# Performance work log

Hardware: AMD Instinct MI355X
Metric: run time of the kernel (lower is better)

Reference implementation:

```python
import jax, jax.numpy as jnp
import numpy as np

K = 2  # top-k experts per token


def setup_inputs() -> dict:
    key = jax.random.key(0)
    k1, k2 = jax.random.split(key)
    B, S, H, E = 4, 4096, 4096, 64
    x = jax.random.normal(k1, (B, S, H), dtype=jnp.float32)
    gate_w = jax.random.normal(k2, (E, H), dtype=jnp.float32) * (H ** -0.5)
    return {"x": x, "gate_w": gate_w}


def reference(x, gate_w):
    # logits = x @ gate_w.T : [B, S, E]
    logits = jnp.einsum("bsh,eh->bse", x, gate_w)
    scores = jax.nn.softmax(logits, axis=-1)
    topk_scores, topk_idx = jax.lax.top_k(scores, K)  # [B, S, K]
    aux_loss = scores.mean() * 0.0
    z_loss = jnp.mean(logits.astype(jnp.float32) ** 2)
    return topk_idx, topk_scores, aux_loss, z_loss
```

## Files before the change

### kernel.cpp

```cpp
#include <hip/hip_runtime.h>
#include <hip/hip_bf16.h>


typedef __bf16  bf16x8  __attribute__((ext_vector_type(8)));
typedef float   f32x16  __attribute__((ext_vector_type(16)));

#define BS_TOK 16384
#define H_DIM  4096
#define E_DIM  64
#define MT     32
#define KWAVE  1024
#define NPANEL 16
#define WS_ZBUF_OFF (1536u << 10)

__device__ __forceinline__ void split3(float v, __bf16 &b0, __bf16 &b1, __bf16 &b2) {
    b0 = (__bf16)v;
    float r = v - (float)b0;
    b1 = (__bf16)r;
    float r2 = r - (float)b1;
    b2 = (__bf16)r2;
}

__device__ __forceinline__ void async_copy16(const float* gp, float* lp) {
    __builtin_amdgcn_global_load_lds(
        (const __attribute__((address_space(1))) void*)gp,
        (__attribute__((address_space(3))) void*)lp, 16, 0, 0);
}

__global__ void prep_w(const float* __restrict__ gw, bf16x8* __restrict__ wb) {
    int idx  = blockIdx.x * blockDim.x + threadIdx.x;
    int kb   = idx >> 7;
    int rem  = idx & 127;
    int nt   = rem >> 6;
    int lane = rem & 63;
    int n  = nt * 32 + (lane & 31);
    int kk = kb * 16 + ((lane >> 5) << 3);
    const float* p = gw + (size_t)n * H_DIM + kk;
    bf16x8 t0, t1, t2;
#pragma unroll
    for (int j = 0; j < 8; ++j) {
        __bf16 a, b, c;
        split3(p[j], a, b, c);
        t0[j] = a; t1[j] = b; t2[j] = c;
    }
    size_t fb = (size_t)(kb * 2 + nt) * 3;
    wb[(fb + 0) * 64 + lane] = t0;
    wb[(fb + 1) * 64 + lane] = t1;
    wb[(fb + 2) * 64 + lane] = t2;
}

__global__ __launch_bounds__(256, 2) void fused_router(
        const float* __restrict__ x, const bf16x8* __restrict__ wb,
        float* __restrict__ out, float* __restrict__ zbuf) {
    __shared__ float lds[16384];
    __shared__ float zsh[4];

    int tid = threadIdx.x;
    int w   = tid >> 6;
    int l   = tid & 63;
    int m0  = blockIdx.x * MT;
    float* sw = &lds[w * 4096];

    const float* gp[8];
#pragma unroll
    for (int r = 0; r < 8; ++r) {
        int g = 4 * r + (l >> 4);
        int c = (l & 15) ^ (g & 15);
        gp[r] = x + (size_t)(m0 + g) * H_DIM + w * KWAVE + c * 4;
    }

    f32x16 acc0, acc1;
#pragma unroll
    for (int r = 0; r < 16; ++r) { acc0[r] = 0.f; acc1[r] = 0.f; }

#pragma unroll
    for (int r = 0; r < 8; ++r) async_copy16(gp[r], sw + r * 256);

    int row = l & 31, half = l >> 5, rsw = row & 15;

    for (int p = 0; p < NPANEL; ++p) {
        __builtin_amdgcn_s_waitcnt(0x0F70);
        if (p + 1 < NPANEL) {
            float* dst = sw + ((p + 1) & 1) * 2048;
#pragma unroll
            for (int r = 0; r < 8; ++r)
                async_copy16(gp[r] + (p + 1) * 64, dst + r * 256);
        }
        const float* sb = sw + (p & 1) * 2048;
#pragma unroll
        for (int kk = 0; kk < 4; ++kk) {
            int c0 = kk * 4 + half * 2;
            float4 xa = *(const float4*)&sb[row * 64 + ((c0 ^ rsw) << 2)];
            float4 xb = *(const float4*)&sb[row * 64 + (((c0 + 1) ^ rsw) << 2)];
            bf16x8 a0, a1, a2;
            float xs[8] = {xa.x, xa.y, xa.z, xa.w, xb.x, xb.y, xb.z, xb.w};
#pragma unroll
            for (int j = 0; j < 8; ++j) {
                __bf16 h0, h1, h2;
                split3(xs[j], h0, h1, h2);
                a0[j] = h0; a1[j] = h1; a2[j] = h2;
            }
            int ks_abs = w * 64 + p * 4 + kk;
            const bf16x8* wp = wb + (size_t)ks_abs * 6 * 64 + l;
            bf16x8 b0 = wp[0*64], b1 = wp[1*64], b2 = wp[2*64];
            bf16x8 b3 = wp[3*64], b4 = wp[4*64], b5 = wp[5*64];
            acc0 = __builtin_amdgcn_mfma_f32_32x32x16_bf16(a0, b0, acc0, 0, 0, 0);
            acc0 = __builtin_amdgcn_mfma_f32_32x32x16_bf16(a1, b0, acc0, 0, 0, 0);
            acc0 = __builtin_amdgcn_mfma_f32_32x32x16_bf16(a2, b0, acc0, 0, 0, 0);
            acc0 = __builtin_amdgcn_mfma_f32_32x32x16_bf16(a0, b1, acc0, 0, 0, 0);
            acc0 = __builtin_amdgcn_mfma_f32_32x32x16_bf16(a1, b1, acc0, 0, 0, 0);
            acc0 = __builtin_amdgcn_mfma_f32_32x32x16_bf16(a0, b2, acc0, 0, 0, 0);
            acc1 = __builtin_amdgcn_mfma_f32_32x32x16_bf16(a0, b3, acc1, 0, 0, 0);
            acc1 = __builtin_amdgcn_mfma_f32_32x32x16_bf16(a1, b3, acc1, 0, 0, 0);
            acc1 = __builtin_amdgcn_mfma_f32_32x32x16_bf16(a2, b3, acc1, 0, 0, 0);
            acc1 = __builtin_amdgcn_mfma_f32_32x32x16_bf16(a0, b4, acc1, 0, 0, 0);
            acc1 = __builtin_amdgcn_mfma_f32_32x32x16_bf16(a1, b4, acc1, 0, 0, 0);
            acc1 = __builtin_amdgcn_mfma_f32_32x32x16_bf16(a0, b5, acc1, 0, 0, 0);
        }
    }

    __syncthreads();
    int col = l & 31;
#pragma unroll
    for (int r = 0; r < 16; ++r) {
        int mm = (r & 3) + ((r >> 2) << 3) + (half << 2);
        lds[w * 2048 + mm * 64 + col]      = acc0[r];
        lds[w * 2048 + mm * 64 + 32 + col] = acc1[r];
    }
    __syncthreads();

    float zacc = 0.f;
    for (int i = 0; i < 8; ++i) {
        int tl = w * 8 + i;
        float lg = lds[tl * 64 + l] + lds[2048 + tl * 64 + l]
                 + lds[4096 + tl * 64 + l] + lds[6144 + tl * 64 + l];
        zacc += lg * lg;

        float m = lg;
#pragma unroll
        for (int off = 32; off; off >>= 1) m = fmaxf(m, __shfl_xor(m, off));
        float e = expf(lg - m);
        float d = e;
#pragma unroll
        for (int off = 32; off; off >>= 1) d += __shfl_xor(d, off);
        float sc = e / d;

        float s1 = sc; int i1 = l;
#pragma unroll
        for (int off = 32; off; off >>= 1) {
            float os = __shfl_xor(s1, off); int oi = __shfl_xor(i1, off);
            if (os > s1 || (os == s1 && oi < i1)) { s1 = os; i1 = oi; }
        }
        float sm = (l == i1) ? -1.0f : sc;
        float s2 = sm; int i2 = l;
#pragma unroll
        for (int off = 32; off; off >>= 1) {
            float os = __shfl_xor(s2, off); int oi = __shfl_xor(i2, off);
            if (os > s2 || (os == s2 && oi < i2)) { s2 = os; i2 = oi; }
        }

        if (l == 0) {
            int t = m0 + tl;
            out[2 * t]                  = (float)i1;
            out[2 * t + 1]              = (float)i2;
            out[2 * BS_TOK + 2 * t]     = s1;
            out[2 * BS_TOK + 2 * t + 1] = s2;
        }
    }
#pragma unroll
    for (int off = 32; off; off >>= 1) zacc += __shfl_xor(zacc, off);
    if (l == 0) zsh[w] = zacc;
    __syncthreads();
    if (tid == 0)
        zbuf[blockIdx.x] = zsh[0] + zsh[1] + zsh[2] + zsh[3];
}

__global__ __launch_bounds__(256) void zreduce(const float* __restrict__ zbuf,
                                               float* __restrict__ out) {
    __shared__ float sh[4];
    int tid = threadIdx.x;
    float s = zbuf[tid] + zbuf[tid + 256];
#pragma unroll
    for (int off = 32; off; off >>= 1) s += __shfl_xor(s, off);
    if ((tid & 63) == 0) sh[tid >> 6] = s;
    __syncthreads();
    if (tid == 0) {
        out[4 * BS_TOK]     = 0.0f;
        out[4 * BS_TOK + 1] = (sh[0] + sh[1] + sh[2] + sh[3])
                              * (1.0f / (float)(BS_TOK * E_DIM));
    }
}

extern "C" void kernel_launch(void* const* d_in, const int* in_sizes, int n_in,
                              void* d_out, int out_size, void* d_ws, size_t ws_size,
                              hipStream_t stream) {
    const float* x  = (const float*)d_in[0];
    const float* gw = (const float*)d_in[1];
    float* out  = (float*)d_out;
    bf16x8* wb  = (bf16x8*)d_ws;
    float*  zbf = (float*)((char*)d_ws + WS_ZBUF_OFF);

    prep_w<<<128, 256, 0, stream>>>(gw, wb);
    fused_router<<<BS_TOK / MT, 256, 0, stream>>>(x, wb, out, zbf);
    zreduce<<<1, 256, 0, stream>>>(zbf, out);
}
```

Before: 410.4 us.

## Halve LDS panel size and software-prefetch weight fragments into registers

The x staging panel shrinks from 64 to 32 floats per row, halving LDS per block (64KB to 32KB) so more blocks can be resident. Weight fragments for the next panel are now loaded into a double-buffered register array (wA/wB) one panel ahead, instead of being loaded from global memory right before the MFMAs. The point is to hide weight-load latency and raise occupancy. The cost is more VGPRs (24 bf16x8 registers) and twice as many waitcnt sync points per wave. The single waitcnt(0x0F70) now also waits on the outstanding weight loads, which may serialize them.

```diff
diff --git a/kernel.cpp b/kernel.cpp
--- a/kernel.cpp
+++ b/kernel.cpp
@@ -10,7 +10,8 @@
 #define E_DIM  64
 #define MT     32
 #define KWAVE  1024
-#define NPANEL 16
+#define PANEL  32
+#define NPANEL (KWAVE / PANEL)
 #define WS_ZBUF_OFF (1536u << 10)
 
 __device__ __forceinline__ void split3(float v, __bf16 &b0, __bf16 &b1, __bf16 &b2) {
@@ -52,20 +53,20 @@
 __global__ __launch_bounds__(256, 2) void fused_router(
         const float* __restrict__ x, const bf16x8* __restrict__ wb,
         float* __restrict__ out, float* __restrict__ zbuf) {
-    __shared__ float lds[16384];
+    __shared__ float lds[8192];
     __shared__ float zsh[4];
 
     int tid = threadIdx.x;
     int w   = tid >> 6;
     int l   = tid & 63;
     int m0  = blockIdx.x * MT;
-    float* sw = &lds[w * 4096];
-
-    const float* gp[8];
-#pragma unroll
-    for (int r = 0; r < 8; ++r) {
-        int g = 4 * r + (l >> 4);
-        int c = (l & 15) ^ (g & 15);
+    float* sw = &lds[w * 2048];
+
+    const float* gp[4];
+#pragma unroll
+    for (int r = 0; r < 4; ++r) {
+        int g = 8 * r + (l >> 3);
+        int c = (l & 7) ^ (g & 7);
         gp[r] = x + (size_t)(m0 + g) * H_DIM + w * KWAVE + c * 4;
     }
 
@@ -73,25 +74,21 @@
 #pragma unroll
     for (int r = 0; r < 16; ++r) { acc0[r] = 0.f; acc1[r] = 0.f; }
 
-#pragma unroll
-    for (int r = 0; r < 8; ++r) async_copy16(gp[r], sw + r * 256);
-
-    int row = l & 31, half = l >> 5, rsw = row & 15;
-
-    for (int p = 0; p < NPANEL; ++p) {
-        __builtin_amdgcn_s_waitcnt(0x0F70);
-        if (p + 1 < NPANEL) {
-            float* dst = sw + ((p + 1) & 1) * 2048;
-#pragma unroll
-            for (int r = 0; r < 8; ++r)
-                async_copy16(gp[r] + (p + 1) * 64, dst + r * 256);
-        }
-        const float* sb = sw + (p & 1) * 2048;
-#pragma unroll
-        for (int kk = 0; kk < 4; ++kk) {
-            int c0 = kk * 4 + half * 2;
-            float4 xa = *(const float4*)&sb[row * 64 + ((c0 ^ rsw) << 2)];
-            float4 xb = *(const float4*)&sb[row * 64 + (((c0 + 1) ^ rsw) << 2)];
+    const bf16x8* wbl = wb + l;
+    auto loadW = [&](int p, bf16x8* wf) {
+        const bf16x8* wp = wbl + (size_t)(w * 64 + p * 2) * 6 * 64;
+#pragma unroll
+        for (int i = 0; i < 12; ++i) wf[i] = wp[i * 64];
+    };
+
+    int row = l & 31, half = l >> 5, rsw = (l & 31) & 7;
+
+    auto compute = [&](const float* sb, const bf16x8* wf) {
+#pragma unroll
+        for (int s = 0; s < 2; ++s) {
+            int c0 = s * 4 + half * 2;
+            float4 xa = *(const float4*)&sb[row * 32 + ((c0 ^ rsw) << 2)];
+            float4 xb = *(const float4*)&sb[row * 32 + (((c0 + 1) ^ rsw) << 2)];
             bf16x8 a0, a1, a2;
             float xs[8] = {xa.x, xa.y, xa.z, xa.w, xb.x, xb.y, xb.z, xb.w};
 #pragma unroll
@@ -100,10 +97,8 @@
                 split3(xs[j], h0, h1, h2);
                 a0[j] = h0; a1[j] = h1; a2[j] = h2;
             }
-            int ks_abs = w * 64 + p * 4 + kk;
-            const bf16x8* wp = wb + (size_t)ks_abs * 6 * 64 + l;
-            bf16x8 b0 = wp[0*64], b1 = wp[1*64], b2 = wp[2*64];
-            bf16x8 b3 = wp[3*64], b4 = wp[4*64], b5 = wp[5*64];
+            bf16x8 b0 = wf[s*6+0], b1 = wf[s*6+1], b2 = wf[s*6+2];
+            bf16x8 b3 = wf[s*6+3], b4 = wf[s*6+4], b5 = wf[s*6+5];
             acc0 = __builtin_amdgcn_mfma_f32_32x32x16_bf16(a0, b0, acc0, 0, 0, 0);
             acc0 = __builtin_amdgcn_mfma_f32_32x32x16_bf16(a1, b0, acc0, 0, 0, 0);
             acc0 = __builtin_amdgcn_mfma_f32_32x32x16_bf16(a2, b0, acc0, 0, 0, 0);
@@ -117,6 +112,28 @@
             acc1 = __builtin_amdgcn_mfma_f32_32x32x16_bf16(a1, b4, acc1, 0, 0, 0);
             acc1 = __builtin_amdgcn_mfma_f32_32x32x16_bf16(a0, b5, acc1, 0, 0, 0);
         }
+    };
+
+    bf16x8 wA[12], wB[12];
+    auto body = [&](int P, bf16x8* WC, bf16x8* WN) {
+        __builtin_amdgcn_s_waitcnt(0x0F70);
+        if (P + 1 < NPANEL) {
+            loadW(P + 1, WN);
+            float* dst = sw + ((P + 1) & 1) * 1024;
+#pragma unroll
+            for (int r = 0; r < 4; ++r)
+                async_copy16(gp[r] + (P + 1) * 32, dst + r * 256);
+        }
+        compute(sw + (P & 1) * 1024, WC);
+    };
+
+#pragma unroll
+    for (int r = 0; r < 4; ++r) async_copy16(gp[r], sw + r * 256);
+    loadW(0, wA);
+
+    for (int p = 0; p < NPANEL; p += 2) {
+        body(p,     wA, wB);
+        body(p + 1, wB, wA);
     }
 
     __syncthreads();
```

Result: no change. 410.3 us (-0.0%).
